# Kernel tuning notes

Hardware: AMD Instinct MI355X
Metric: run time of the kernel (lower is better)

## Reference

```python
import jax, jax.numpy as jnp
import numpy as np

IN_F, OUT_F, RANK, ALPHA = 4096, 4096, 8, 32.0

def setup_inputs() -> dict:
    key = jax.random.key(0)
    kx, kw, ka, kb, kbias = jax.random.split(key, 5)
    x = jax.random.normal(kx, (4, 2048, IN_F), dtype=jnp.float32)
    weight = jax.random.normal(kw, (OUT_F, IN_F), dtype=jnp.float32) * 0.02
    a = jax.random.normal(ka, (OUT_F, RANK), dtype=jnp.float32) * 0.02
    b = jax.random.normal(kb, (RANK, IN_F), dtype=jnp.float32) * 0.02  # zeros in init; use randn for nontrivial test
    bias = jax.random.normal(kbias, (OUT_F,), dtype=jnp.float32) * 0.02
    return {"x": x, "weight": weight, "a": a, "b": b, "bias": bias}

def reference(x, weight, a, b, bias):
    # F.linear(x, W, bias) + F.linear(x, a @ b) * alpha / r
    base = jnp.einsum('bsi,oi->bso', x, weight) + bias
    # low-rank path computed in factored form (same math as x @ (a@b).T)
    lora = jnp.einsum('bsr,or->bso', jnp.einsum('bsi,ri->bsr', x, b), a)
    return base + lora * (ALPHA / RANK)
```

## Files before the change

### kernel.cpp

```cpp
#include <hip/hip_runtime.h>
#include <stdint.h>

#define IN_F 4096
#define OUT_F 4096
#define M_TOT 8192
#define LORA_SCALE 4.0f

typedef unsigned short u16;
typedef __attribute__((ext_vector_type(8))) short bf16x8;
typedef __attribute__((ext_vector_type(4))) float f32x4;

__device__ __forceinline__ u16 f2bf(float f) {
  union { float f; unsigned u; } v; v.f = f;
  unsigned r = v.u + 0x7FFFu + ((v.u >> 16) & 1u);
  return (u16)(r >> 16);
}

__device__ __forceinline__ void gload_lds16(const void* g, void* l) {
  __builtin_amdgcn_global_load_lds(
      (const __attribute__((address_space(1))) void*)g,
      (__attribute__((address_space(3))) void*)l, 16, 0, 0);
}

__global__ void prep(const float* __restrict__ X, const float* __restrict__ W,
                     const float* __restrict__ A, const float* __restrict__ B,
                     u16* __restrict__ Xb, u16* __restrict__ Wb) {
  int bid = blockIdx.x;
  if (bid < 16384) {
    size_t base = ((size_t)bid * blockDim.x + threadIdx.x) * 8;
    const f32x4* p = (const f32x4*)(X + base);
    f32x4 v0 = __builtin_nontemporal_load(p);
    f32x4 v1 = __builtin_nontemporal_load(p + 1);
    uint4 pk;
    pk.x = (unsigned)f2bf(v0.x) | ((unsigned)f2bf(v0.y) << 16);
    pk.y = (unsigned)f2bf(v0.z) | ((unsigned)f2bf(v0.w) << 16);
    pk.z = (unsigned)f2bf(v1.x) | ((unsigned)f2bf(v1.y) << 16);
    pk.w = (unsigned)f2bf(v1.z) | ((unsigned)f2bf(v1.w) << 16);
    *(uint4*)(Xb + base) = pk;
  } else {
    int idx = (bid - 16384) * blockDim.x + threadIdx.x;
    int o  = idx >> 10;
    int i0 = (idx & 1023) << 2;
    const f32x4 w = __builtin_nontemporal_load((const f32x4*)(W + (size_t)o * IN_F + i0));
    float a0 = w.x, a1 = w.y, a2 = w.z, a3 = w.w;
#pragma unroll
    for (int r = 0; r < 8; ++r) {
      float ar = A[o * 8 + r] * LORA_SCALE;
      const float4 bv = *(const float4*)(B + (size_t)r * IN_F + i0);
      a0 += ar * bv.x; a1 += ar * bv.y; a2 += ar * bv.z; a3 += ar * bv.w;
    }
    uint2 pk;
    pk.x = (unsigned)f2bf(a0) | ((unsigned)f2bf(a1) << 16);
    pk.y = (unsigned)f2bf(a2) | ((unsigned)f2bf(a3) << 16);
    *(uint2*)(Wb + (size_t)o * IN_F + i0) = pk;
  }
}


#define ABASE(b) ((b) * 32768)
#define BBASE(b) ((b) * 32768 + 16384)

#define STAGE_A(b, h, kt) do { \
  gload_lds16(aG + (size_t)((h) * 128) * IN_F + (kt),      lds + ABASE(b) + ((h) * 128) * 64      + tid * 8); \
  gload_lds16(aG + (size_t)((h) * 128 + 64) * IN_F + (kt), lds + ABASE(b) + ((h) * 128 + 64) * 64 + tid * 8); \
} while (0)

#define STAGE_B(b, h, kt) do { \
  gload_lds16(bG + (size_t)((h) * 128) * IN_F + (kt),      lds + BBASE(b) + ((h) * 128) * 64      + tid * 8); \
  gload_lds16(bG + (size_t)((h) * 128 + 64) * IN_F + (kt), lds + BBASE(b) + ((h) * 128 + 64) * 64 + tid * 8); \
} while (0)

#define WAIT4 asm volatile("s_waitcnt vmcnt(4)" ::: "memory")
#define WAIT0 asm volatile("s_waitcnt vmcnt(0)" ::: "memory")
#define DRAIN asm volatile("s_waitcnt lgkmcnt(0)" ::: "memory")

#define MFMA16 __builtin_amdgcn_mfma_f32_16x16x32_bf16

#define PHASE16(b, mh, s, STAGE_STMT, TAIL_STMT) do { \
  __builtin_amdgcn_s_barrier(); \
  __builtin_amdgcn_sched_barrier(0); \
  if ((s) == 0 && (mh) == 0) { \
    _Pragma("unroll") \
    for (int n = 0; n < 4; ++n) \
      Bf0[n] = *(const bf16x8*)(lds + BBASE(b) + (rB + n * 16) * 64 + ck0); \
  } \
  if ((s) == 0 && (mh) == 1) { \
    _Pragma("unroll") \
    for (int n = 0; n < 4; ++n) \
      Bf1[n] = *(const bf16x8*)(lds + BBASE(b) + (rB + n * 16) * 64 + ck1); \
  } \
  bf16x8 a_[4]; \
  _Pragma("unroll") \
  for (int j = 0; j < 4; ++j) \
    a_[j] = *(const bf16x8*)(lds + ABASE(b) + (rA + (mh) * 64 + j * 16) * 64 + ((s) ? ck1 : ck0)); \
  STAGE_STMT; \
  __builtin_amdgcn_s_setprio(1); \
  _Pragma("unroll") \
  for (int j = 0; j < 4; ++j) \
    _Pragma("unroll") \
    for (int n = 0; n < 4; ++n) \
      acc[(mh) * 4 + j][n] = MFMA16(a_[j], ((s) ? Bf1 : Bf0)[n], acc[(mh) * 4 + j][n], 0, 0, 0); \
  __builtin_amdgcn_s_setprio(0); \
  TAIL_STMT; \
} while (0)

__global__ __launch_bounds__(512, 2) void gemm8(const u16* __restrict__ Xb,
                                                const u16* __restrict__ Wb,
                                                const float* __restrict__ bias,
                                                float* __restrict__ out) {
  extern __shared__ u16 lds[];

  const int tid  = threadIdx.x;
  const int lane = tid & 63;
  const int wid  = tid >> 6;
  const int wr = wid >> 2, wc = wid & 3;
  const int lr = lane & 15, kg = lane >> 4;

  const int bid = blockIdx.x;
  const int swz = (bid & 7) * 64 + (bid >> 3);
  const int mt = swz >> 4, nt = swz & 15;
  const int m0 = mt * 256, n0 = nt * 256;

  const int srow = tid >> 3;
  const int swc  = (tid & 7) ^ (srow & 7);
  const u16* aG = Xb + (size_t)(m0 + srow) * IN_F + swc * 8;
  const u16* bG = Wb + (size_t)(n0 + srow) * IN_F + swc * 8;

  const int rA = wr * 128 + lr;
  const int rB = wc * 64 + lr;
  const int ck0 = ((kg) ^ (lane & 7)) * 8;
  const int ck1 = ((4 + kg) ^ (lane & 7)) * 8;

  f32x4 acc[8][4] = {};
  bf16x8 Bf0[4], Bf1[4];

  STAGE_B(0, 0, 0); STAGE_B(0, 1, 0);
  STAGE_A(0, 0, 0); STAGE_A(0, 1, 0);
  STAGE_B(1, 0, 64); STAGE_B(1, 1, 64);
  WAIT4;

  for (int i = 0; i < 31; ++i) {
    const int kt1 = i * 128 + 64, kt2 = i * 128 + 128, kt3 = i * 128 + 192;
    PHASE16(0, 0, 0, STAGE_A(1, 0, kt1), );
    PHASE16(0, 1, 0, STAGE_A(1, 1, kt1), DRAIN);
    PHASE16(0, 0, 1, STAGE_B(0, 0, kt2), );
    PHASE16(0, 1, 1, STAGE_B(0, 1, kt2), WAIT4);
    PHASE16(1, 0, 0, STAGE_A(0, 0, kt2), );
    PHASE16(1, 1, 0, STAGE_A(0, 1, kt2), DRAIN);
    PHASE16(1, 0, 1, STAGE_B(1, 0, kt3), );
    PHASE16(1, 1, 1, STAGE_B(1, 1, kt3), WAIT4);
  }
  PHASE16(0, 0, 0, STAGE_A(1, 0, 4032), );
  PHASE16(0, 1, 0, STAGE_A(1, 1, 4032), DRAIN);
  PHASE16(0, 0, 1, , );
  PHASE16(0, 1, 1, , WAIT0);
  PHASE16(1, 0, 0, , );
  PHASE16(1, 1, 0, , );
  PHASE16(1, 0, 1, , );
  PHASE16(1, 1, 1, , );

  float bv[4];
#pragma unroll
  for (int n = 0; n < 4; ++n) bv[n] = bias[n0 + wc * 64 + n * 16 + lr];
  const int rbase = m0 + wr * 128 + kg * 4;
#pragma unroll
  for (int m = 0; m < 8; ++m)
#pragma unroll
    for (int n = 0; n < 4; ++n) {
      int col = n0 + wc * 64 + n * 16 + lr;
#pragma unroll
      for (int r = 0; r < 4; ++r)
        __builtin_nontemporal_store(acc[m][n][r] + bv[n],
                                    &out[(size_t)(rbase + m * 16 + r) * OUT_F + col]);
    }
}

__global__ __launch_bounds__(256) void gemm_bias(const u16* __restrict__ Xb,
                                                 const u16* __restrict__ Wb,
                                                 const float* __restrict__ bias,
                                                 float* __restrict__ out) {
  __shared__ __align__(16) u16 ldsA[128 * 64];
  __shared__ __align__(16) u16 ldsB[128 * 64];

  const int tid  = threadIdx.x;
  const int wid  = tid >> 6;
  const int lane = tid & 63;
  const int nt = blockIdx.x & 31;
  const int mt = blockIdx.x >> 5;
  const int m0 = mt * 128, n0 = nt * 128;
  const int wr = wid >> 1, wc = wid & 1;
  const int lr = lane & 15;
  const int kg = lane >> 4;

  const int srow   = wid * 8 + (lane >> 3);
  const int schunk = (lane & 7) ^ (srow & 7);
  const u16* aSrc = Xb + (size_t)(m0 + srow) * IN_F + schunk * 8;
  const u16* bSrc = Wb + (size_t)(n0 + srow) * IN_F + schunk * 8;

  f32x4 acc[4][4] = {};

  for (int kt = 0; kt < IN_F; kt += 64) {
    __syncthreads();
#pragma unroll
    for (int j = 0; j < 4; ++j) {
      gload_lds16(aSrc + (size_t)(j * 32) * IN_F + kt, &ldsA[j * 2048 + wid * 512]);
      gload_lds16(bSrc + (size_t)(j * 32) * IN_F + kt, &ldsB[j * 2048 + wid * 512]);
    }
    __syncthreads();

#pragma unroll
    for (int s = 0; s < 2; ++s) {
      bf16x8 af[4], bfr[4];
#pragma unroll
      for (int m = 0; m < 4; ++m) {
        int r = wr * 64 + m * 16 + lr;
        int c = (s * 4 + kg) ^ (r & 7);
        af[m] = *(const bf16x8*)&ldsA[r * 64 + c * 8];
      }
#pragma unroll
      for (int n = 0; n < 4; ++n) {
        int r = wc * 64 + n * 16 + lr;
        int c = (s * 4 + kg) ^ (r & 7);
        bfr[n] = *(const bf16x8*)&ldsB[r * 64 + c * 8];
      }
#pragma unroll
      for (int m = 0; m < 4; ++m)
#pragma unroll
        for (int n = 0; n < 4; ++n)
          acc[m][n] = __builtin_amdgcn_mfma_f32_16x16x32_bf16(af[m], bfr[n], acc[m][n], 0, 0, 0);
    }
  }

  float bv[4];
#pragma unroll
  for (int n = 0; n < 4; ++n) bv[n] = bias[n0 + wc * 64 + n * 16 + lr];
  const int rbase = m0 + wr * 64 + kg * 4;
#pragma unroll
  for (int m = 0; m < 4; ++m)
#pragma unroll
    for (int n = 0; n < 4; ++n) {
      int col = n0 + wc * 64 + n * 16 + lr;
#pragma unroll
      for (int r = 0; r < 4; ++r)
        out[(size_t)(rbase + m * 16 + r) * OUT_F + col] = acc[m][n][r] + bv[n];
    }
}

__global__ void lora_t(const float* __restrict__ x, const float* __restrict__ B,
                       float* __restrict__ t) {
  int m = blockIdx.x;
  int tid = threadIdx.x, lane = tid & 63;
  float p[8] = {0, 0, 0, 0, 0, 0, 0, 0};
  for (int k = tid; k < IN_F; k += 256) {
    float xv = x[(size_t)m * IN_F + k];
#pragma unroll
    for (int r = 0; r < 8; ++r) p[r] += xv * B[r * IN_F + k];
  }
#pragma unroll
  for (int r = 0; r < 8; ++r) {
    float v = p[r];
    for (int off = 32; off; off >>= 1) v += __shfl_down(v, off);
    if (lane == 0) atomicAdd(&t[m * 8 + r], v);
  }
}

__global__ void fb_gemm(const float* __restrict__ x, const float* __restrict__ W,
                        const float* __restrict__ A, const float* __restrict__ bias,
                        const float* __restrict__ t, float* __restrict__ out) {
  __shared__ float sx[64][17];
  __shared__ float sw[64][17];
  int tx = threadIdx.x, ty = threadIdx.y;
  int tid = ty * 16 + tx;
  int m0 = blockIdx.y * 64, n0 = blockIdx.x * 64;
  float acc[4][4] = {};
  for (int kt = 0; kt < IN_F; kt += 16) {
    __syncthreads();
#pragma unroll
    for (int q = 0; q < 4; ++q) {
      int idx = q * 256 + tid;
      int r = idx >> 4, c = idx & 15;
      sx[r][c] = x[(size_t)(m0 + r) * IN_F + kt + c];
      sw[r][c] = W[(size_t)(n0 + r) * IN_F + kt + c];
    }
    __syncthreads();
#pragma unroll
    for (int k = 0; k < 16; ++k) {
      float xv[4], wv[4];
#pragma unroll
      for (int i = 0; i < 4; ++i) xv[i] = sx[ty * 4 + i][k];
#pragma unroll
      for (int j = 0; j < 4; ++j) wv[j] = sw[tx * 4 + j][k];
#pragma unroll
      for (int i = 0; i < 4; ++i)
#pragma unroll
        for (int j = 0; j < 4; ++j) acc[i][j] += xv[i] * wv[j];
    }
  }
#pragma unroll
  for (int i = 0; i < 4; ++i) {
    int m = m0 + ty * 4 + i;
    float tv[8];
#pragma unroll
    for (int r = 0; r < 8; ++r) tv[r] = t[m * 8 + r];
#pragma unroll
    for (int j = 0; j < 4; ++j) {
      int o = n0 + tx * 4 + j;
      float lora = 0.f;
#pragma unroll
      for (int r = 0; r < 8; ++r) lora += tv[r] * A[o * 8 + r];
      out[(size_t)m * OUT_F + o] = acc[i][j] + bias[o] + LORA_SCALE * lora;
    }
  }
}

extern "C" void kernel_launch(void* const* d_in, const int* in_sizes, int n_in,
                              void* d_out, int out_size, void* d_ws, size_t ws_size,
                              hipStream_t stream) {
  const float* x    = (const float*)d_in[0];
  const float* W    = (const float*)d_in[1];
  const float* A    = (const float*)d_in[2];
  const float* B    = (const float*)d_in[3];
  const float* bias = (const float*)d_in[4];
  float* out = (float*)d_out;

  const size_t xb_elems = (size_t)M_TOT * IN_F;
  const size_t wb_elems = (size_t)OUT_F * IN_F;
  const size_t need = (xb_elems + wb_elems) * sizeof(u16);

  if (ws_size >= need) {
    u16* Xb = (u16*)d_ws;
    u16* Wb = Xb + xb_elems;
    prep<<<32768, 256, 0, stream>>>(x, W, A, B, Xb, Wb);

    hipError_t e = hipFuncSetAttribute((const void*)gemm8,
                                       hipFuncAttributeMaxDynamicSharedMemorySize,
                                       131072);
    bool used8 = false;
    if (e == hipSuccess) {
      gemm8<<<512, 512, 131072, stream>>>(Xb, Wb, bias, out);
      used8 = (hipGetLastError() == hipSuccess);
    }
    if (!used8) {
      gemm_bias<<<(M_TOT / 128) * (OUT_F / 128), 256, 0, stream>>>(Xb, Wb, bias, out);
    }
  } else {
    float* t = (float*)d_ws;
    (void)hipMemsetAsync(t, 0, (size_t)M_TOT * 8 * sizeof(float), stream);
    lora_t<<<M_TOT, 256, 0, stream>>>(x, B, t);
    fb_gemm<<<dim3(OUT_F / 64, M_TOT / 64), dim3(16, 16), 0, stream>>>(x, W, A, bias, t, out);
  }
}
```

Baseline: 296.0 us.

## Merge M-half phases into full K-half phases with fewer barriers

Restructures the gemm8 main loop so each phase loads all 8 A fragments and 4 B fragments for one K-half and issues 32 MFMAs, instead of splitting into two M-halves with separate barriers. Staging of the next tile moves after the MFMA block, and the explicit LDS drain waits are removed. This halves the number of barriers and phase overheads per K-tile, at the cost of more live VGPRs for A fragments and less interleaving of global-to-LDS loads with compute.

```diff
diff --git a/kernel.cpp b/kernel.cpp
--- a/kernel.cpp
+++ b/kernel.cpp
@@ -72,36 +72,26 @@
 
 #define WAIT4 asm volatile("s_waitcnt vmcnt(4)" ::: "memory")
 #define WAIT0 asm volatile("s_waitcnt vmcnt(0)" ::: "memory")
-#define DRAIN asm volatile("s_waitcnt lgkmcnt(0)" ::: "memory")
 
 #define MFMA16 __builtin_amdgcn_mfma_f32_16x16x32_bf16
 
-#define PHASE16(b, mh, s, STAGE_STMT, TAIL_STMT) do { \
+#define KHALF(b, s, TAIL_STAGE) do { \
   __builtin_amdgcn_s_barrier(); \
   __builtin_amdgcn_sched_barrier(0); \
-  if ((s) == 0 && (mh) == 0) { \
+  _Pragma("unroll") \
+  for (int n = 0; n < 4; ++n) \
+    Bf[n] = *(const bf16x8*)(lds + BBASE(b) + (rB + n * 16) * 64 + ((s) ? ck1 : ck0)); \
+  _Pragma("unroll") \
+  for (int m = 0; m < 8; ++m) \
+    Af[m] = *(const bf16x8*)(lds + ABASE(b) + (rA + m * 16) * 64 + ((s) ? ck1 : ck0)); \
+  __builtin_amdgcn_s_setprio(1); \
+  _Pragma("unroll") \
+  for (int m = 0; m < 8; ++m) \
     _Pragma("unroll") \
     for (int n = 0; n < 4; ++n) \
-      Bf0[n] = *(const bf16x8*)(lds + BBASE(b) + (rB + n * 16) * 64 + ck0); \
-  } \
-  if ((s) == 0 && (mh) == 1) { \
-    _Pragma("unroll") \
-    for (int n = 0; n < 4; ++n) \
-      Bf1[n] = *(const bf16x8*)(lds + BBASE(b) + (rB + n * 16) * 64 + ck1); \
-  } \
-  bf16x8 a_[4]; \
-  _Pragma("unroll") \
-  for (int j = 0; j < 4; ++j) \
-    a_[j] = *(const bf16x8*)(lds + ABASE(b) + (rA + (mh) * 64 + j * 16) * 64 + ((s) ? ck1 : ck0)); \
-  STAGE_STMT; \
-  __builtin_amdgcn_s_setprio(1); \
-  _Pragma("unroll") \
-  for (int j = 0; j < 4; ++j) \
-    _Pragma("unroll") \
-    for (int n = 0; n < 4; ++n) \
-      acc[(mh) * 4 + j][n] = MFMA16(a_[j], ((s) ? Bf1 : Bf0)[n], acc[(mh) * 4 + j][n], 0, 0, 0); \
+      acc[m][n] = MFMA16(Af[m], Bf[n], acc[m][n], 0, 0, 0); \
   __builtin_amdgcn_s_setprio(0); \
-  TAIL_STMT; \
+  TAIL_STAGE; \
 } while (0)
 
 __global__ __launch_bounds__(512, 2) void gemm8(const u16* __restrict__ Xb,
@@ -132,7 +122,7 @@
   const int ck1 = ((4 + kg) ^ (lane & 7)) * 8;
 
   f32x4 acc[8][4] = {};
-  bf16x8 Bf0[4], Bf1[4];
+  bf16x8 Af[8], Bf[4];
 
   STAGE_B(0, 0, 0); STAGE_B(0, 1, 0);
   STAGE_A(0, 0, 0); STAGE_A(0, 1, 0);
@@ -141,23 +131,18 @@
 
   for (int i = 0; i < 31; ++i) {
     const int kt1 = i * 128 + 64, kt2 = i * 128 + 128, kt3 = i * 128 + 192;
-    PHASE16(0, 0, 0, STAGE_A(1, 0, kt1), );
-    PHASE16(0, 1, 0, STAGE_A(1, 1, kt1), DRAIN);
-    PHASE16(0, 0, 1, STAGE_B(0, 0, kt2), );
-    PHASE16(0, 1, 1, STAGE_B(0, 1, kt2), WAIT4);
-    PHASE16(1, 0, 0, STAGE_A(0, 0, kt2), );
-    PHASE16(1, 1, 0, STAGE_A(0, 1, kt2), DRAIN);
-    PHASE16(1, 0, 1, STAGE_B(1, 0, kt3), );
-    PHASE16(1, 1, 1, STAGE_B(1, 1, kt3), WAIT4);
-  }
-  PHASE16(0, 0, 0, STAGE_A(1, 0, 4032), );
-  PHASE16(0, 1, 0, STAGE_A(1, 1, 4032), DRAIN);
-  PHASE16(0, 0, 1, , );
-  PHASE16(0, 1, 1, , WAIT0);
-  PHASE16(1, 0, 0, , );
-  PHASE16(1, 1, 0, , );
-  PHASE16(1, 0, 1, , );
-  PHASE16(1, 1, 1, , );
+    KHALF(0, 0, STAGE_A(1, 0, kt1); STAGE_A(1, 1, kt1));
+    KHALF(0, 1, STAGE_B(0, 0, kt2); STAGE_B(0, 1, kt2));
+    WAIT4;
+    KHALF(1, 0, STAGE_A(0, 0, kt2); STAGE_A(0, 1, kt2));
+    KHALF(1, 1, STAGE_B(1, 0, kt3); STAGE_B(1, 1, kt3));
+    WAIT4;
+  }
+  KHALF(0, 0, STAGE_A(1, 0, 4032); STAGE_A(1, 1, 4032));
+  KHALF(0, 1, );
+  WAIT0;
+  KHALF(1, 0, );
+  KHALF(1, 1, );
 
   float bv[4];
 #pragma unroll
```

Result: no change. 292.6 us (-1.2%).
